# Kernel optimization log

Hardware: AMD Instinct MI355X
Metric: run time of the kernel (lower is better)

## Reference

```python
import jax, jax.numpy as jnp
import numpy as np

N_NODES = 100000
N_EDGES = 3200000
NFEAT = 256
NHID = 256


def setup_inputs() -> dict:
    key = jax.random.key(0)
    k_x, k_ws, k_wn, k_src, k_dst = jax.random.split(key, 5)
    x = jax.random.normal(k_x, (N_NODES, NFEAT), dtype=jnp.float32)
    W_self = jax.random.normal(k_ws, (NFEAT, NHID), dtype=jnp.float32) * (1.0 / np.sqrt(NFEAT))
    W_neigh = jax.random.normal(k_wn, (NFEAT, NHID), dtype=jnp.float32) * (1.0 / np.sqrt(NFEAT))
    b = jnp.zeros((NHID,), dtype=jnp.float32)
    edge_src = jax.random.randint(k_src, (N_EDGES,), 0, N_NODES, dtype=jnp.int32)
    edge_dst = jax.random.randint(k_dst, (N_EDGES,), 0, N_NODES, dtype=jnp.int32)
    return {"x": x, "W_self": W_self, "W_neigh": W_neigh, "b": b,
            "edge_src": edge_src, "edge_dst": edge_dst}


def reference(x, W_self, W_neigh, b, edge_src, edge_dst):
    n = x.shape[0]
    # mean aggregation over incoming edges: gather src feats, scatter-add to dst
    msg = x[edge_src]                                              # [E, F]
    agg = jax.ops.segment_sum(msg, edge_dst, num_segments=n)       # [N, F]
    deg = jax.ops.segment_sum(jnp.ones_like(edge_dst, dtype=x.dtype),
                              edge_dst, num_segments=n)            # [N]
    h_neigh = agg / jnp.maximum(deg, 1.0)[:, None]                 # mean (0 for isolated)
    # SAGEConv 'mean': fc_self(x) + fc_neigh(h_neigh) (bias on neigh branch)
    out = x @ W_self + h_neigh @ W_neigh + b                       # [N, H]
    return jax.nn.relu(out)
```

## Files before the change

### kernel.cpp

```cpp
#include <hip/hip_runtime.h>
#include <stdint.h>

typedef __attribute__((ext_vector_type(8))) short bf16x8;
typedef __attribute__((ext_vector_type(4))) float f32x4;
typedef __attribute__((ext_vector_type(2))) float f32x2;

#define NF 256
#define NH 256
#define KTOT 512
#define BM 128
#define BN 128
#define BK 64
#define EB 512
#define NBIN 512

static __device__ __forceinline__ unsigned short f2bf(float f){
  union { float f; unsigned int u; } v; v.f = f;
  unsigned int r = v.u + 0x7fffu + ((v.u >> 16) & 1u);
  return (unsigned short)(r >> 16);
}
static __device__ __forceinline__ unsigned int f2e4(float f){
  union { float f; unsigned int u; } v; v.f = f;
  unsigned int s = v.u >> 31;
  unsigned int mag = v.u & 0x7fffffffu;
  if (mag > 0x43E00000u) mag = 0x43E00000u;
  unsigned int r = mag + 0x7ffffu + ((mag >> 20) & 1u);
  if (r < 0x3C800000u) return 0u;
  return (s << 7) | (((r >> 20) - 960u) & 0x7fu);
}
static __device__ __forceinline__ ushort4 dec8(unsigned int v){
#if __has_builtin(__builtin_amdgcn_cvt_pk_f32_fp8)
  f32x2 lo = __builtin_amdgcn_cvt_pk_f32_fp8((int)v, false);
  f32x2 hi = __builtin_amdgcn_cvt_pk_f32_fp8((int)v, true);
  ushort4 o; o.x=f2bf(lo[0]); o.y=f2bf(lo[1]); o.z=f2bf(hi[0]); o.w=f2bf(hi[1]);
  return o;
#else
  ushort4 o; unsigned short r[4];
  #pragma unroll
  for (int j = 0; j < 4; j++){
    unsigned int b = (v >> (8*j)) & 0xffu;
    unsigned int tt = b & 0x7fu;
    union { unsigned int u; float f; } w;
    w.u = ((tt + 960u) << 20) | ((b & 0x80u) << 24);
    r[j] = tt ? f2bf(w.f) : (unsigned short)0;
  }
  o.x=r[0]; o.y=r[1]; o.z=r[2]; o.w=r[3];
  return o;
#endif
}
static __device__ __forceinline__ void accw(unsigned int v, f32x2& a, f32x2& b){
#if __has_builtin(__builtin_amdgcn_cvt_pk_f32_fp8)
  a += __builtin_amdgcn_cvt_pk_f32_fp8((int)v, false);
  b += __builtin_amdgcn_cvt_pk_f32_fp8((int)v, true);
#else
  #pragma unroll
  for (int j = 0; j < 4; j++){
    unsigned int bb = (v >> (8*j)) & 0xffu;
    unsigned int tt = bb & 0x7fu;
    union { unsigned int u; float f; } w;
    w.u = ((tt + 960u) << 20) | ((bb & 0x80u) << 24);
    float f = tt ? w.f : 0.f;
    if (j==0) a[0] += f; else if (j==1) a[1] += f; else if (j==2) b[0] += f; else b[1] += f;
  }
#endif
}
static __device__ __forceinline__ unsigned int pkw(f32x2 a, f32x2 b){
#if __has_builtin(__builtin_amdgcn_cvt_pk_fp8_f32)
  int t = __builtin_amdgcn_cvt_pk_fp8_f32(a[0], a[1], 0, false);
  t = __builtin_amdgcn_cvt_pk_fp8_f32(b[0], b[1], t, true);
  return (unsigned int)t;
#else
  return f2e4(a[0]) | (f2e4(a[1])<<8) | (f2e4(b[0])<<16) | (f2e4(b[1])<<24);
#endif
}
static __device__ __forceinline__ void gload16(const void* g, void* lds_wave_base, int lane){
#if __has_builtin(__builtin_amdgcn_global_load_lds)
  __builtin_amdgcn_global_load_lds(
      (const __attribute__((address_space(1))) unsigned int*)g,
      (__attribute__((address_space(3))) unsigned int*)lds_wave_base, 16, 0, 0);
  (void)lane;
#else
  *(int4*)((char*)lds_wave_base + (size_t)lane*16) = *(const int4*)g;
#endif
}

__global__ void k_cvt_x(const float* __restrict__ x, unsigned short* __restrict__ xb,
                        unsigned int* __restrict__ xq, int n8){
  for (int i = blockIdx.x*blockDim.x + threadIdx.x; i < n8; i += gridDim.x*blockDim.x){
    const float4* p = (const float4*)(x + (size_t)i*8);
    float4 a = p[0], b = p[1];
    ushort4 o0, o1;
    o0.x=f2bf(a.x); o0.y=f2bf(a.y); o0.z=f2bf(a.z); o0.w=f2bf(a.w);
    o1.x=f2bf(b.x); o1.y=f2bf(b.y); o1.z=f2bf(b.z); o1.w=f2bf(b.w);
    ushort4* q = (ushort4*)(xb + (size_t)i*8);
    q[0] = o0; q[1] = o1;
    unsigned int w0 = f2e4(a.x) | (f2e4(a.y)<<8) | (f2e4(a.z)<<16) | (f2e4(a.w)<<24);
    unsigned int w1 = f2e4(b.x) | (f2e4(b.y)<<8) | (f2e4(b.z)<<16) | (f2e4(b.w)<<24);
    uint2 o; o.x = w0; o.y = w1;
    ((uint2*)xq)[i] = o;
  }
}

__global__ void k_cvt_w(const float* __restrict__ Ws, const float* __restrict__ Wn,
                        unsigned short* __restrict__ Wt){
  int t = blockIdx.x*blockDim.x + threadIdx.x;
  if (t >= NH*KTOT) return;
  int n = t >> 9, k = t & 511;
  float v = (k < NF) ? Ws[(size_t)k*NH + n] : Wn[(size_t)(k-NF)*NH + n];
  Wt[t] = (unsigned short)f2bf(v);
}

__global__ void __launch_bounds__(256) k_bhist(const int* __restrict__ dst,
                                               int* __restrict__ H, int ne){
  __shared__ int lh[NBIN];
  int blk = blockIdx.x, t = threadIdx.x;
  for (int i = t; i < NBIN; i += 256) lh[i] = 0;
  __syncthreads();
  int chunk = (ne + EB - 1) / EB;
  int e0 = blk * chunk, e1 = ne < e0 + chunk ? ne : e0 + chunk;
  for (int e = e0 + t; e < e1; e += 256)
    atomicAdd(&lh[((unsigned)dst[e]) >> 8], 1);
  __syncthreads();
  for (int i = t; i < NBIN; i += 256) H[i*EB + blk] = lh[i];
}

__global__ void k_partial(const int* __restrict__ deg, int* __restrict__ partial, int n){
  __shared__ int sm[256];
  int b = blockIdx.x, t = threadIdx.x;
  int i0 = b*1024 + t*4;
  int s = 0;
  if (i0 + 3 < n){ int4 v = *(const int4*)(deg + i0); s = v.x+v.y+v.z+v.w; }
  else { for (int j=0;j<4;j++) if (i0+j < n) s += deg[i0+j]; }
  sm[t] = s; __syncthreads();
  for (int d = 128; d > 0; d >>= 1){ if (t < d) sm[t] += sm[t+d]; __syncthreads(); }
  if (t == 0) partial[b] = sm[0];
}

__global__ void k_scanp(int* __restrict__ partial, int nb){
  __shared__ int sm[256];
  int t = threadIdx.x;
  int v = (t < nb) ? partial[t] : 0;
  sm[t] = v; __syncthreads();
  for (int d = 1; d < 256; d <<= 1){
    int u = (t >= d) ? sm[t-d] : 0; __syncthreads();
    sm[t] += u; __syncthreads();
  }
  if (t < nb) partial[t] = sm[t] - v;
}

__global__ void k_scanapply(const int* __restrict__ deg, const int* __restrict__ partial,
                            int* __restrict__ off, int n, int ne){
  __shared__ int sm[256];
  int b = blockIdx.x, t = threadIdx.x;
  int i0 = b*1024 + t*4;
  int d0=0,d1=0,d2=0,d3=0;
  if (i0 + 3 < n){ int4 v = *(const int4*)(deg + i0); d0=v.x; d1=v.y; d2=v.z; d3=v.w; }
  else { if(i0<n)d0=deg[i0]; if(i0+1<n)d1=deg[i0+1]; if(i0+2<n)d2=deg[i0+2]; if(i0+3<n)d3=deg[i0+3]; }
  int s = d0+d1+d2+d3;
  sm[t] = s; __syncthreads();
  for (int d = 1; d < 256; d <<= 1){
    int u = (t >= d) ? sm[t-d] : 0; __syncthreads();
    sm[t] += u; __syncthreads();
  }
  int run = partial[b] + sm[t] - s;
  if (i0   < n) off[i0]   = run; run += d0;
  if (i0+1 < n) off[i0+1] = run; run += d1;
  if (i0+2 < n) off[i0+2] = run; run += d2;
  if (i0+3 < n) off[i0+3] = run;
  if (b == 0 && t == 0) off[n] = ne;
}

__global__ void __launch_bounds__(256) k_bscat(const int* __restrict__ src,
                                               const int* __restrict__ dst,
                                               const int* __restrict__ base,
                                               unsigned int* __restrict__ bkt, int ne){
  __shared__ int lc[NBIN];
  __shared__ int lb[NBIN];
  int blk = blockIdx.x, t = threadIdx.x;
  for (int i = t; i < NBIN; i += 256){ lc[i] = 0; lb[i] = base[i*EB + blk]; }
  __syncthreads();
  int chunk = (ne + EB - 1) / EB;
  int e0 = blk * chunk, e1 = ne < e0 + chunk ? ne : e0 + chunk;
  for (int e = e0 + t; e < e1; e += 256){
    int d = dst[e];
    int bin = ((unsigned)d) >> 8;
    int p = lb[bin] + atomicAdd(&lc[bin], 1);
    bkt[p] = (((unsigned)src[e]) << 8) | ((unsigned)d & 255u);
  }
}

__global__ void __launch_bounds__(256) k_csr(const unsigned int* __restrict__ bkt,
                                             const int* __restrict__ base,
                                             int* __restrict__ off, int* __restrict__ col,
                                             int nn, int ne){
  __shared__ int lh[256], sc[256], se[256], lc[256];
  int b = blockIdx.x, t = threadIdx.x;
  int n0 = base[b*EB], n1 = base[(b+1)*EB];
  lh[t] = 0; lc[t] = 0;
  __syncthreads();
  for (int e = n0 + t; e < n1; e += 256)
    atomicAdd(&lh[bkt[e] & 255u], 1);
  __syncthreads();
  int v = lh[t];
  sc[t] = v; __syncthreads();
  for (int d = 1; d < 256; d <<= 1){
    int u = (t >= d) ? sc[t-d] : 0; __syncthreads();
    sc[t] += u; __syncthreads();
  }
  int excl = sc[t] - v;
  se[t] = excl;
  int node = b*256 + t;
  if (node <= nn) off[node] = n0 + excl;
  __syncthreads();
  for (int e = n0 + t; e < n1; e += 256){
    unsigned u = bkt[e];
    int low = (int)(u & 255u);
    int r = atomicAdd(&lc[low], 1);
    col[n0 + se[low] + r] = (int)(u >> 8);
  }
}

__global__ void __launch_bounds__(256) k_agg(const unsigned int* __restrict__ xw,
                                             const int* __restrict__ off,
                                             const int* __restrict__ col,
                                             unsigned int* __restrict__ hq, int n){
  int w = threadIdx.x >> 6;
  int lane = threadIdx.x & 63;
  int node = blockIdx.x*4 + w;
  if (node >= n) return;
  int e0 = off[node], e1 = off[node+1];
  int deg = e1 - e0;
  f32x2 alo = (f32x2){0.f,0.f}, ahi = (f32x2){0.f,0.f};
  for (int c0 = 0; c0 < deg; c0 += 64){
    int len = deg - c0; if (len > 64) len = 64;
    int cv = 0;
    if (lane < len) cv = col[e0 + c0 + lane];
    int i = 0;
    for (; i + 16 <= len; i += 16){
      unsigned int u[16];
      #pragma unroll
      for (int j = 0; j < 16; j++){
        int s = __builtin_amdgcn_readlane(cv, i + j);
        u[j] = xw[(size_t)s*64 + lane];
      }
      #pragma unroll
      for (int j = 0; j < 16; j++) accw(u[j], alo, ahi);
    }
    for (; i + 4 <= len; i += 4){
      unsigned int u[4];
      #pragma unroll
      for (int j = 0; j < 4; j++){
        int s = __builtin_amdgcn_readlane(cv, i + j);
        u[j] = xw[(size_t)s*64 + lane];
      }
      #pragma unroll
      for (int j = 0; j < 4; j++) accw(u[j], alo, ahi);
    }
    for (; i < len; ++i){
      int s = __builtin_amdgcn_readlane(cv, i);
      unsigned int u0 = xw[(size_t)s*64 + lane];
      accw(u0, alo, ahi);
    }
  }
  float inv = 1.f / (float)(deg > 1 ? deg : 1);
  alo *= inv; ahi *= inv;
  hq[(size_t)node*64 + lane] = pkw(alo, ahi);
}

__global__ void __launch_bounds__(256) k_gemm(const unsigned short* __restrict__ xb,
                                              const unsigned char*  __restrict__ hq,
                                              const unsigned short* __restrict__ Wt,
                                              const float* __restrict__ bias,
                                              float* __restrict__ out, int M){
  __shared__ __align__(16) unsigned short As[BM*BK];
  __shared__ __align__(16) unsigned short Bs[BN*BK];
  int t = threadIdx.x;
  int n0 = blockIdx.x * BN;
  int m0 = blockIdx.y * BM;
  int w = t >> 6, lane = t & 63;
  int wm = w >> 1, wn = w & 1;
  int lrow = lane & 15;
  int cgrp = (lane >> 4) * 16;
  int row_s = t >> 3;
  int slot  = t & 7;

  f32x4 acc[4][4];
  #pragma unroll
  for (int i=0;i<4;i++)
    #pragma unroll
    for (int j=0;j<4;j++) acc[i][j] = (f32x4){0.f,0.f,0.f,0.f};

  for (int kk = 0; kk < KTOT; kk += BK){
    __syncthreads();
    if (kk < NF){
      #pragma unroll
      for (int r = 0; r < 4; r++){
        int row = r*32 + row_s;
        const char* g = (const char*)(xb + (size_t)(m0 + row)*NF + kk)
                        + ((slot ^ (row & 7)) << 4);
        gload16(g, (char*)As + (size_t)(r*256 + (t & ~63))*16, lane);
      }
    } else {
      #pragma unroll
      for (int r = 0; r < 4; r++){
        int row = r*32 + row_s;
        const unsigned char* g = hq + (size_t)(m0 + row)*NF + (kk - NF)
                                 + ((slot ^ (row & 7)) << 3);
        uint2 v = *(const uint2*)g;
        ushort4 lo = dec8(v.x), hi = dec8(v.y);
        char* dstb = (char*)As + (size_t)row*128 + slot*16;
        *(ushort4*)dstb = lo;
        *(ushort4*)(dstb + 8) = hi;
      }
    }
    #pragma unroll
    for (int r = 0; r < 4; r++){
      int row = r*32 + row_s;
      const char* g = (const char*)(Wt + (size_t)(n0 + row)*KTOT + kk)
                      + ((slot ^ (row & 7)) << 4);
      gload16(g, (char*)Bs + (size_t)(r*256 + (t & ~63))*16, lane);
    }
    __syncthreads();

    #pragma unroll
    for (int ks = 0; ks < 2; ks++){
      bf16x8 af[4], bfr[4];
      #pragma unroll
      for (int mi=0;mi<4;mi++){
        int row = wm*64 + mi*16 + lrow;
        int cb = (ks*64 + cgrp) ^ ((row & 7) << 4);
        af[mi] = *(const bf16x8*)((const char*)As + (size_t)row*128 + cb);
      }
      #pragma unroll
      for (int ni=0;ni<4;ni++){
        int row = wn*64 + ni*16 + lrow;
        int cb = (ks*64 + cgrp) ^ ((row & 7) << 4);
        bfr[ni] = *(const bf16x8*)((const char*)Bs + (size_t)row*128 + cb);
      }
      #pragma unroll
      for (int mi=0;mi<4;mi++)
        #pragma unroll
        for (int ni=0;ni<4;ni++)
          acc[mi][ni] = __builtin_amdgcn_mfma_f32_16x16x32_bf16(af[mi], bfr[ni], acc[mi][ni], 0, 0, 0);
    }
  }

  #pragma unroll
  for (int ni=0;ni<4;ni++){
    int cn = n0 + wn*64 + ni*16 + lrow;
    float bv = bias[cn];
    #pragma unroll
    for (int mi=0;mi<4;mi++){
      #pragma unroll
      for (int r=0;r<4;r++){
        int rm = m0 + wm*64 + mi*16 + (lane>>4)*4 + r;
        if (rm < M){
          float v = acc[mi][ni][r] + bv;
          out[(size_t)rm*NH + cn] = v > 0.f ? v : 0.f;
        }
      }
    }
  }
}

extern "C" void kernel_launch(void* const* d_in, const int* in_sizes, int n_in,
                              void* d_out, int out_size, void* d_ws, size_t ws_size,
                              hipStream_t stream){
  const float* x      = (const float*)d_in[0];
  const float* Wself  = (const float*)d_in[1];
  const float* Wneigh = (const float*)d_in[2];
  const float* bias   = (const float*)d_in[3];
  const int*   esrc   = (const int*)d_in[4];
  const int*   edst   = (const int*)d_in[5];
  const int nn = in_sizes[0] / NF;
  const int ne = in_sizes[4];
  const int mpad = ((nn + BM - 1) / BM) * BM;

  char* w = (char*)d_ws;
  auto alloc = [&](size_t bytes)->char*{
    char* p = w; w += (bytes + 511) & ~size_t(511); return p;
  };
  unsigned short* xb  = (unsigned short*)alloc((size_t)mpad*NF*2);
  unsigned char*  xq  = (unsigned char*)alloc((size_t)nn*NF);
  char* hq_bkt        = alloc((size_t)mpad*NF);
  int* col            = (int*)alloc((size_t)ne*4);
  int* base           = (int*)alloc(((size_t)NBIN*EB + 1)*4);
  int* off            = (int*)alloc((size_t)(nn+1)*4);
  unsigned short* Wt  = (unsigned short*)alloc((size_t)NH*KTOT*2);
  int* partial        = (int*)alloc(4096);
  unsigned int* bkt   = (unsigned int*)hq_bkt;
  unsigned char* hq   = (unsigned char*)hq_bkt;
  int* H              = col;

  const int nH = NBIN*EB;
  const int nb = nH / 1024;

  k_cvt_x<<<2048, 256, 0, stream>>>(x, xb, (unsigned int*)xq, nn*NF/8);
  k_cvt_w<<<(NH*KTOT + 255)/256, 256, 0, stream>>>(Wself, Wneigh, Wt);
  k_bhist<<<EB, 256, 0, stream>>>(edst, H, ne);
  k_partial<<<nb, 256, 0, stream>>>(H, partial, nH);
  k_scanp<<<1, 256, 0, stream>>>(partial, nb);
  k_scanapply<<<nb, 256, 0, stream>>>(H, partial, base, nH, ne);
  k_bscat<<<EB, 256, 0, stream>>>(esrc, edst, base, bkt, ne);
  k_csr<<<NBIN, 256, 0, stream>>>(bkt, base, off, col, nn, ne);
  k_agg<<<(nn + 3)/4, 256, 0, stream>>>((const unsigned int*)xq, off, col, (unsigned int*)hq, nn);
  dim3 gg(NH/BN, mpad/BM);
  k_gemm<<<gg, 256, 0, stream>>>(xb, hq, Wt, bias, (float*)d_out, nn);
}
```

Measured before the change: 323.1 us.

## Widen GEMM tile to full output width and merge conversion kernels

The GEMM now uses 512-thread blocks, each covering all 256 output columns for a 128-row tile. Each A tile, including the fp8-decoded neighbour tile, is loaded and decoded once instead of twice, which halves A traffic and decode work. The x and weight conversion kernels are also fused into one launch to drop a kernel launch. In exchange, each block needs more LDS (48KB) and has fewer blocks in flight, which may reduce occupancy and latency hiding.

```diff
diff --git a/kernel.cpp b/kernel.cpp
--- a/kernel.cpp
+++ b/kernel.cpp
@@ -9,7 +9,6 @@
 #define NH 256
 #define KTOT 512
 #define BM 128
-#define BN 128
 #define BK 64
 #define EB 512
 #define NBIN 512
@@ -84,30 +83,32 @@
 #endif
 }
 
-__global__ void k_cvt_x(const float* __restrict__ x, unsigned short* __restrict__ xb,
-                        unsigned int* __restrict__ xq, int n8){
-  for (int i = blockIdx.x*blockDim.x + threadIdx.x; i < n8; i += gridDim.x*blockDim.x){
-    const float4* p = (const float4*)(x + (size_t)i*8);
-    float4 a = p[0], b = p[1];
-    ushort4 o0, o1;
-    o0.x=f2bf(a.x); o0.y=f2bf(a.y); o0.z=f2bf(a.z); o0.w=f2bf(a.w);
-    o1.x=f2bf(b.x); o1.y=f2bf(b.y); o1.z=f2bf(b.z); o1.w=f2bf(b.w);
-    ushort4* q = (ushort4*)(xb + (size_t)i*8);
-    q[0] = o0; q[1] = o1;
-    unsigned int w0 = f2e4(a.x) | (f2e4(a.y)<<8) | (f2e4(a.z)<<16) | (f2e4(a.w)<<24);
-    unsigned int w1 = f2e4(b.x) | (f2e4(b.y)<<8) | (f2e4(b.z)<<16) | (f2e4(b.w)<<24);
-    uint2 o; o.x = w0; o.y = w1;
-    ((uint2*)xq)[i] = o;
-  }
-}
-
-__global__ void k_cvt_w(const float* __restrict__ Ws, const float* __restrict__ Wn,
-                        unsigned short* __restrict__ Wt){
-  int t = blockIdx.x*blockDim.x + threadIdx.x;
-  if (t >= NH*KTOT) return;
-  int n = t >> 9, k = t & 511;
-  float v = (k < NF) ? Ws[(size_t)k*NH + n] : Wn[(size_t)(k-NF)*NH + n];
-  Wt[t] = (unsigned short)f2bf(v);
+__global__ void k_cvt(const float* __restrict__ x, unsigned short* __restrict__ xb,
+                      unsigned int* __restrict__ xq, int n8,
+                      const float* __restrict__ Ws, const float* __restrict__ Wn,
+                      unsigned short* __restrict__ Wt){
+  if (blockIdx.x < 2048){
+    for (int i = blockIdx.x*blockDim.x + threadIdx.x; i < n8; i += 2048*blockDim.x){
+      const float4* p = (const float4*)(x + (size_t)i*8);
+      float4 a = p[0], b = p[1];
+      ushort4 o0, o1;
+      o0.x=f2bf(a.x); o0.y=f2bf(a.y); o0.z=f2bf(a.z); o0.w=f2bf(a.w);
+      o1.x=f2bf(b.x); o1.y=f2bf(b.y); o1.z=f2bf(b.z); o1.w=f2bf(b.w);
+      ushort4* q = (ushort4*)(xb + (size_t)i*8);
+      q[0] = o0; q[1] = o1;
+      unsigned int w0 = f2e4(a.x) | (f2e4(a.y)<<8) | (f2e4(a.z)<<16) | (f2e4(a.w)<<24);
+      unsigned int w1 = f2e4(b.x) | (f2e4(b.y)<<8) | (f2e4(b.z)<<16) | (f2e4(b.w)<<24);
+      uint2 o; o.x = w0; o.y = w1;
+      ((uint2*)xq)[i] = o;
+    }
+  } else {
+    int t = (blockIdx.x - 2048)*blockDim.x + threadIdx.x;
+    if (t < NH*KTOT){
+      int n = t >> 9, k = t & 511;
+      float v = (k < NF) ? Ws[(size_t)k*NH + n] : Wn[(size_t)(k-NF)*NH + n];
+      Wt[t] = (unsigned short)f2bf(v);
+    }
+  }
 }
 
 __global__ void __launch_bounds__(256) k_bhist(const int* __restrict__ dst,
@@ -267,21 +268,19 @@
   hq[(size_t)node*64 + lane] = pkw(alo, ahi);
 }
 
-__global__ void __launch_bounds__(256) k_gemm(const unsigned short* __restrict__ xb,
-                                              const unsigned char*  __restrict__ hq,
-                                              const unsigned short* __restrict__ Wt,
-                                              const float* __restrict__ bias,
-                                              float* __restrict__ out, int M){
+__global__ void __launch_bounds__(512, 4) k_gemm(const unsigned short* __restrict__ xb,
+                                                 const unsigned char*  __restrict__ hq,
+                                                 const unsigned short* __restrict__ Wt,
+                                                 const float* __restrict__ bias,
+                                                 float* __restrict__ out, int M){
   __shared__ __align__(16) unsigned short As[BM*BK];
-  __shared__ __align__(16) unsigned short Bs[BN*BK];
+  __shared__ __align__(16) unsigned short Bs[NH*BK];
   int t = threadIdx.x;
-  int n0 = blockIdx.x * BN;
-  int m0 = blockIdx.y * BM;
+  int m0 = blockIdx.x * BM;
   int w = t >> 6, lane = t & 63;
-  int wm = w >> 1, wn = w & 1;
+  int wm = w >> 2, wn = w & 3;
   int lrow = lane & 15;
   int cgrp = (lane >> 4) * 16;
-  int row_s = t >> 3;
   int slot  = t & 7;
 
   f32x4 acc[4][4];
@@ -294,16 +293,18 @@
     __syncthreads();
     if (kk < NF){
       #pragma unroll
-      for (int r = 0; r < 4; r++){
-        int row = r*32 + row_s;
+      for (int p = 0; p < 2; p++){
+        int flat = p*512 + t;
+        int row = flat >> 3;
         const char* g = (const char*)(xb + (size_t)(m0 + row)*NF + kk)
                         + ((slot ^ (row & 7)) << 4);
-        gload16(g, (char*)As + (size_t)(r*256 + (t & ~63))*16, lane);
+        gload16(g, (char*)As + (size_t)(flat & ~63)*16, lane);
       }
     } else {
       #pragma unroll
-      for (int r = 0; r < 4; r++){
-        int row = r*32 + row_s;
+      for (int p = 0; p < 2; p++){
+        int flat = p*512 + t;
+        int row = flat >> 3;
         const unsigned char* g = hq + (size_t)(m0 + row)*NF + (kk - NF)
                                  + ((slot ^ (row & 7)) << 3);
         uint2 v = *(const uint2*)g;
@@ -314,11 +315,12 @@
       }
     }
     #pragma unroll
-    for (int r = 0; r < 4; r++){
-      int row = r*32 + row_s;
-      const char* g = (const char*)(Wt + (size_t)(n0 + row)*KTOT + kk)
+    for (int q = 0; q < 4; q++){
+      int flat = q*512 + t;
+      int row = flat >> 3;
+      const char* g = (const char*)(Wt + (size_t)row*KTOT + kk)
                       + ((slot ^ (row & 7)) << 4);
-      gload16(g, (char*)Bs + (size_t)(r*256 + (t & ~63))*16, lane);
+      gload16(g, (char*)Bs + (size_t)(flat & ~63)*16, lane);
     }
     __syncthreads();
 
@@ -347,7 +349,7 @@
 
   #pragma unroll
   for (int ni=0;ni<4;ni++){
-    int cn = n0 + wn*64 + ni*16 + lrow;
+    int cn = wn*64 + ni*16 + lrow;
     float bv = bias[cn];
     #pragma unroll
     for (int mi=0;mi<4;mi++){
@@ -395,8 +397,7 @@
   const int nH = NBIN*EB;
   const int nb = nH / 1024;
 
-  k_cvt_x<<<2048, 256, 0, stream>>>(x, xb, (unsigned int*)xq, nn*NF/8);
-  k_cvt_w<<<(NH*KTOT + 255)/256, 256, 0, stream>>>(Wself, Wneigh, Wt);
+  k_cvt<<<2048 + 512, 256, 0, stream>>>(x, xb, (unsigned int*)xq, nn*NF/8, Wself, Wneigh, Wt);
   k_bhist<<<EB, 256, 0, stream>>>(edst, H, ne);
   k_partial<<<nb, 256, 0, stream>>>(H, partial, nH);
   k_scanp<<<1, 256, 0, stream>>>(partial, nb);
@@ -404,6 +405,5 @@
   k_bscat<<<EB, 256, 0, stream>>>(esrc, edst, base, bkt, ne);
   k_csr<<<NBIN, 256, 0, stream>>>(bkt, base, off, col, nn, ne);
   k_agg<<<(nn + 3)/4, 256, 0, stream>>>((const unsigned int*)xq, off, col, (unsigned int*)hq, nn);
-  dim3 gg(NH/BN, mpad/BM);
-  k_gemm<<<gg, 256, 0, stream>>>(xb, hq, Wt, bias, (float*)d_out, nn);
-}
+  k_gemm<<<mpad/BM, 512, 0, stream>>>(xb, hq, Wt, bias, (float*)d_out, nn);
+}
```

After: 308.6 us. 1.05x faster.
